# Performance work log

Hardware: AMD Instinct MI355X
Metric: run time of the kernel (lower is better)

The kernel has to match this reference:

```python
import jax, jax.numpy as jnp
import numpy as np

V, E, H = 100000, 300, 256          # pretrained vectors, emb_dim, rep_dim
B, QLEN, DOC, S = 32, 32, 2048, 64  # batch, max_query_len, max_doc_len, max_num_sent
L = DOC // S                        # sentence length (lengths sum exactly to DOC)
VOCAB = V + 2                       # + extra token + padding idx


def _uniform(k, shape, scale):
    return jax.random.uniform(k, shape, jnp.float32, -scale, scale)


def setup_inputs() -> dict:
    key = jax.random.key(0)
    ks = jax.random.split(key, 16)
    s = 1.0 / np.sqrt(H)  # PyTorch GRU default init scale
    return {
        "queries": jax.random.randint(ks[0], (B, QLEN), 0, V),
        "query_lengths": jax.random.randint(ks[1], (B,), QLEN // 2, QLEN + 1).astype(jnp.int32),
        "docs": jax.random.randint(ks[2], (B, DOC), 0, V),
        "sentence_lengths": jnp.full((B, S), L, dtype=jnp.int32),
        "emb": jax.random.normal(ks[3], (VOCAB, E), jnp.float32) * 0.1,
        "q_wih": _uniform(ks[4], (3 * H, E), s), "q_whh": _uniform(ks[5], (3 * H, H), s),
        "q_bih": _uniform(ks[6], (3 * H,), s), "q_bhh": _uniform(ks[7], (3 * H,), s),
        "f_wih": _uniform(ks[8], (3 * H, E), s), "f_whh": _uniform(ks[9], (3 * H, H), s),
        "f_bih": _uniform(ks[10], (3 * H,), s), "f_bhh": _uniform(ks[11], (3 * H,), s),
        "b_wih": _uniform(ks[12], (3 * H, E), s), "b_whh": _uniform(ks[13], (3 * H, H), s),
        "b_bih": _uniform(ks[14], (3 * H,), s), "b_bhh": _uniform(ks[15], (3 * H,), s),
    }


def _gru(x, wih, whh, bih, bhh, reverse=False):
    # x: (B, T, E) -> hidden states (B, T, H); PyTorch GRU cell equations.
    xg = jnp.einsum('bte,ge->btg', x, wih) + bih  # (B, T, 3H) input projections

    def step(h, xt):
        gh = h @ whh.T + bhh
        ir, iz, inn = jnp.split(xt, 3, axis=-1)
        hr, hz, hn = jnp.split(gh, 3, axis=-1)
        r = jax.nn.sigmoid(ir + hr)
        z = jax.nn.sigmoid(iz + hz)
        n = jnp.tanh(inn + r * hn)
        hnew = (1.0 - z) * n + z * h
        return hnew, hnew

    h0 = jnp.zeros((x.shape[0], whh.shape[1]), x.dtype)
    _, hs = jax.lax.scan(step, h0, jnp.swapaxes(xg, 0, 1), reverse=reverse)
    return jnp.swapaxes(hs, 0, 1)


def reference(queries, query_lengths, docs, sentence_lengths, emb,
              q_wih, q_whh, q_bih, q_bhh,
              f_wih, f_whh, f_bih, f_bhh,
              b_wih, b_whh, b_bih, b_bhh):
    q_emb = emb[queries]  # (B, QLEN, E)
    d_emb = emb[docs]     # (B, DOC, E)

    # Ragged per-sentence mean pooling (_get_facts) as one segment-mean per doc.
    def seg_mean(xb, lens):
        ids = jnp.repeat(jnp.arange(S), lens, total_repeat_length=DOC)
        sums = jax.ops.segment_sum(xb, ids, num_segments=S)
        return sums / jnp.maximum(lens, 1)[:, None].astype(xb.dtype)

    facts = jax.vmap(seg_mean)(d_emb, sentence_lengths)  # (B, S, E)

    # Question GRU: hidden state at the last valid token (pack_padded semantics).
    q_hs = _gru(q_emb, q_wih, q_whh, q_bih, q_bhh)
    q_rep = q_hs[jnp.arange(B), query_lengths - 1][:, None, :]  # (B, 1, H)

    # Input fusion: bidirectional GRU over facts, fwd + bwd halves summed (dropout off / eval).
    f_out = (_gru(facts, f_wih, f_whh, f_bih, f_bhh)
             + _gru(facts, b_wih, b_whh, b_bih, b_bhh, reverse=True))  # (B, S, H)

    num_facts = jnp.sum(sentence_lengths > 0, axis=1)
    return q_rep, f_out, num_facts
```

## Files before the change

kernel.cpp:

```cpp
#include <hip/hip_runtime.h>

#define Bn   32
#define QL   32
#define DOCn 2048
#define Sn   64
#define En   300
#define Hn   256

typedef short bf16x8 __attribute__((ext_vector_type(8)));
typedef short s16x4  __attribute__((ext_vector_type(4)));
typedef float f32x4  __attribute__((ext_vector_type(4)));

static __device__ __forceinline__ float b2f(short s){
  unsigned int u = ((unsigned int)(unsigned short)s) << 16;
  float f; __builtin_memcpy(&f, &u, 4); return f;
}
static __device__ __forceinline__ short f2b(float f){
  unsigned int u; __builtin_memcpy(&u, &f, 4);
  u = u + 0x7fffu + ((u >> 16) & 1u);
  return (short)(u >> 16);
}
static __device__ __forceinline__ float sigm(float x){ return 1.0f/(1.0f+__expf(-x)); }
static __device__ __forceinline__ float tanhx(float x){ return 1.0f - 2.0f/(__expf(2.0f*x)+1.0f); }
static __device__ __forceinline__ f32x4 mfma16(bf16x8 a, bf16x8 b, f32x4 c){
  return __builtin_amdgcn_mfma_f32_16x16x32_bf16(a, b, c, 0, 0, 0);
}
static __device__ __forceinline__ void bar_lgkm(){
  asm volatile("s_waitcnt lgkmcnt(0)\n\ts_barrier" ::: "memory");
}

__global__ __launch_bounds__(256) void k_facts(
    const int* __restrict__ docs, const int* __restrict__ slens,
    const float* __restrict__ emb,
    const float* __restrict__ f_wih, const float* __restrict__ b_wih,
    const float* __restrict__ q_wih,
    short* __restrict__ facts, short* __restrict__ wcvt,
    float* __restrict__ dout)
{
  const int tid = threadIdx.x;

  if (blockIdx.x >= 2048){
    const int rg0 = (blockIdx.x - 2048)*8;
#pragma unroll
    for (int rr = 0; rr < 8; ++rr){
      const int rg = rg0 + rr;
      const int z = rg / 768, g = rg % 768;
      const float* src = ((z == 0) ? f_wih : (z == 1) ? b_wih : q_wih) + (long)g*En;
      short* dst = wcvt + (long)rg*320;
      for (int c = tid; c < 320; c += 256)
        dst[c] = (c < En) ? f2b(src[c]) : (short)0;
    }
    return;
  }

  __shared__ int pref[2*Sn];
  const int blk = blockIdx.x;
  const int b = blk >> 6, s = blk & 63;
  if (tid < Sn){
    const int v = slens[b*Sn + tid];
    int x = v;
#pragma unroll
    for (int d = 1; d < 64; d <<= 1){
      const int y = __shfl_up(x, d, 64);
      if (tid >= d) x += y;
    }
    pref[tid] = x - v;
    pref[Sn + tid] = v;
    if (s == 0){
      const unsigned long long m = __ballot(v > 0);
      if (tid == 0) dout[Bn*Hn + (long)Bn*Sn*Hn + b] = (float)__popcll(m);
    }
  }
  __syncthreads();
  const int off = pref[s];
  const int len = pref[Sn + s];
  const bool act = tid < 150;
  float a0 = 0.f, a1 = 0.f, b0 = 0.f, b1 = 0.f;
  const int* dtok = docs + b*DOCn + off;
  int tkA = (0 < len) ? dtok[0] : 0;
  int tkB = (1 < len) ? dtok[1] : 0;
  int i = 0;
  for (; i + 2 <= len; i += 2){
    const int tkA2 = (i+2 < len) ? dtok[i+2] : 0;
    const int tkB2 = (i+3 < len) ? dtok[i+3] : 0;
    if (act){
      const float2 va = *(const float2*)(emb + (long)tkA*En + 2*tid);
      const float2 vb = *(const float2*)(emb + (long)tkB*En + 2*tid);
      a0 += va.x; a1 += va.y; b0 += vb.x; b1 += vb.y;
    }
    tkA = tkA2; tkB = tkB2;
  }
  if (i < len && act){
    const float2 va = *(const float2*)(emb + (long)tkA*En + 2*tid);
    a0 += va.x; a1 += va.y;
  }
  a0 += b0; a1 += b1;
  const float inv = 1.0f / (float)(len > 0 ? len : 1);
  short* frow = facts + ((long)b*Sn + s)*320;
  if (act){
    frow[2*tid]   = f2b(a0*inv);
    frow[2*tid+1] = f2b(a1*inv);
  } else if (tid < 160){
    const int e = tid - 150;
    frow[300 + 2*e] = 0; frow[301 + 2*e] = 0;
  }
}

__global__ __launch_bounds__(256) void k_xg(
    const short* __restrict__ facts, const short* __restrict__ wcvt,
    const int* __restrict__ queries, const float* __restrict__ emb,
    const float* __restrict__ q_bih, const float* __restrict__ q_bhh,
    const float* __restrict__ f_bih, const float* __restrict__ f_bhh,
    const float* __restrict__ b_bih, const float* __restrict__ b_bhh,
    short* __restrict__ q_xgi, short* __restrict__ f_xgi,
    short* __restrict__ b_xgi)
{
  const int z = blockIdx.z;
  const int bm = blockIdx.x, bn = blockIdx.y;
  const bool isq = (z == 2);
  if (isq && bm >= 8) return;

  const float* bih = (z == 0) ? f_bih : (z == 1) ? b_bih : q_bih;
  const float* bhh = (z == 0) ? f_bhh : (z == 1) ? b_bhh : q_bhh;
  short*       xgi = (z == 0) ? f_xgi : (z == 1) ? b_xgi : q_xgi;

  __shared__ alignas(16) short Al[2][128][40];
  const int tid = threadIdx.x;
  const int l = tid & 63, w = tid >> 6;
  const int wm = w & 1, wn = w >> 1;
  const int l15 = l & 15, lq = l >> 4;
  const int ak8 = w*8;

  bf16x8 bfr[2][10];
#pragma unroll
  for (int nt = 0; nt < 2; ++nt){
    const int g = bn*64 + wn*32 + nt*16 + l15;
    const short* wr = wcvt + ((long)z*768 + g)*320;
#pragma unroll
    for (int kk = 0; kk < 10; ++kk)
      bfr[nt][kk] = *(const bf16x8*)&wr[kk*32 + lq*8];
  }

  const short* asrc_f0 = nullptr; const short* asrc_f1 = nullptr;
  const float* asrc_q0 = nullptr; const float* asrc_q1 = nullptr;
  if (isq){
    asrc_q0 = emb + (long)queries[bm*128 + l]*En;
    asrc_q1 = emb + (long)queries[bm*128 + 64 + l]*En;
  } else {
    asrc_f0 = facts + (long)(bm*128 + l)*320;
    asrc_f1 = facts + (long)(bm*128 + 64 + l)*320;
  }

  bf16x8 va0, va1;
#define LDA_(KK) do{ const int k0_ = (KK)*32 + ak8; \
    if (!isq){ \
      va0 = *(const bf16x8*)(asrc_f0 + k0_); \
      va1 = *(const bf16x8*)(asrc_f1 + k0_); \
    } else if (k0_ + 7 < En){ \
      const f32x4 p0 = *(const f32x4*)(asrc_q0+k0_), p1 = *(const f32x4*)(asrc_q0+k0_+4); \
      const f32x4 p2 = *(const f32x4*)(asrc_q1+k0_), p3 = *(const f32x4*)(asrc_q1+k0_+4); \
      _Pragma("unroll") for (int j = 0; j < 4; ++j){ \
        va0[j] = f2b(p0[j]); va0[4+j] = f2b(p1[j]); \
        va1[j] = f2b(p2[j]); va1[4+j] = f2b(p3[j]); } \
    } else { \
      _Pragma("unroll") for (int j = 0; j < 8; ++j){ const int k_ = k0_ + j; \
        va0[j] = (k_ < En) ? f2b(asrc_q0[k_]) : (short)0; \
        va1[j] = (k_ < En) ? f2b(asrc_q1[k_]) : (short)0; } \
    } }while(0)
#define STA_(BUF) do{ *(bf16x8*)&Al[BUF][l][ak8] = va0; \
    *(bf16x8*)&Al[BUF][64 + l][ak8] = va1; }while(0)

  LDA_(0); STA_(0);
  __syncthreads();

  f32x4 acc[4][2] = {};
#pragma unroll
  for (int kk = 0; kk < 10; ++kk){
    if (kk < 9) LDA_(kk+1);
#pragma unroll
    for (int mt = 0; mt < 4; ++mt){
      bf16x8 a = *(const bf16x8*)&Al[kk&1][wm*64 + mt*16 + l15][lq*8];
      acc[mt][0] = mfma16(a, bfr[0][kk], acc[mt][0]);
      acc[mt][1] = mfma16(a, bfr[1][kk], acc[mt][1]);
    }
    if (kk < 9) STA_((kk+1)&1);
    __syncthreads();
  }
#undef LDA_
#undef STA_

#pragma unroll
  for (int nt = 0; nt < 2; ++nt){
    const int cg = bn*64 + wn*32 + nt*16 + l15;
    float bias = bih[cg];
    if (cg < 512) bias += bhh[cg];
    const int gate = cg >> 8, hc = cg & 255;
    const int wslot = (hc >> 4)*64 + (hc & 15);
#pragma unroll
    for (int mt = 0; mt < 4; ++mt){
      const int r0 = bm*128 + wm*64 + mt*16 + lq*4;
#pragma unroll
      for (int p = 0; p < 4; ++p){
        const int r = r0 + p;
        const int t_ = isq ? (r & 31) : (r & 63);
        const int b_ = isq ? (r >> 5) : (r >> 6);
        const int mh_ = b_ >> 4, rb = b_ & 15;
        const long sidx = (long)t_*32768 + mh_*16384
                        + (long)(wslot + (rb >> 2)*16)*16 + (rb & 3)*3 + gate;
        xgi[sidx] = f2b(acc[mt][nt][p] + bias);
      }
    }
  }
}

__global__ __launch_bounds__(1024) void k_gru(
    const short* __restrict__ q_xg, const short* __restrict__ f_xg,
    const short* __restrict__ b_xg,
    const float* __restrict__ q_whh, const float* __restrict__ q_bhh,
    const float* __restrict__ f_whh, const float* __restrict__ f_bhh,
    const float* __restrict__ b_whh, const float* __restrict__ b_bhh,
    const int* __restrict__ qlens,
    float* __restrict__ dout)
{
  __shared__ alignas(16) short hl[2*16*264];
  __shared__ alignas(16) short wl[7*1024*8];

  const int gru = blockIdx.x >> 1;
  const int mh  = blockIdx.x & 1;
  const int tid = threadIdx.x;
  const int l = tid & 63, w = tid >> 6;
  const int l15 = l & 15, lq = l >> 4;

  const float* whh = (gru == 0) ? q_whh : (gru == 1) ? f_whh : b_whh;
  const float* bhh = (gru == 0) ? q_bhh : (gru == 1) ? f_bhh : b_bhh;
  const short* xgp = (gru == 0) ? q_xg  : (gru == 1) ? f_xg  : b_xg;
  const int T = (gru == 0) ? QL : Sn;

  const int c = w*16 + l15;

  bf16x8 wf[3][6];
  float bhn = 0.f;
#pragma unroll
  for (int gi = 0; gi < 3; ++gi){
    const int g = gi*256 + c;
    const float* wr = whh + (long)g*Hn;
#pragma unroll
    for (int kk = 0; kk < 8; ++kk){
      const f32x4 f0 = *(const f32x4*)(wr + kk*32 + lq*8);
      const f32x4 f1 = *(const f32x4*)(wr + kk*32 + lq*8 + 4);
      bf16x8 v;
#pragma unroll
      for (int j = 0; j < 4; ++j){ v[j] = f2b(f0[j]); v[4+j] = f2b(f1[j]); }
      if (kk < 5 || (kk == 5 && gi < 2)) wf[gi][kk] = v;
      else if (kk == 5)                  *(bf16x8*)&wl[(6*1024 + tid)*8] = v;
      else                               *(bf16x8*)&wl[(((kk-6)*3 + gi)*1024 + tid)*8] = v;
    }
    if (gi == 2) bhn = bhh[g];
  }

  float hreg[4] = {};
  int qlen_m[4];
#pragma unroll
  for (int p = 0; p < 4; ++p) qlen_m[p] = (gru == 0) ? qlens[mh*16 + lq*4 + p] : -1;

  const int so = mh*16384 + tid*16;
  float* qdst  = dout + (mh*16 + lq*4)*Hn + c;
  float* fbase = dout + Bn*Hn + (long)(mh*16 + lq*4)*(Sn*Hn) + c;

  bf16x8 preA0, preA1, preB0, preB1;

#define TOF(TT) ((gru == 2) ? (T - 1 - (TT)) : (TT))
#define LOADP(P0, P1, TI) do{ const short* sb_ = xgp + (long)(TI)*32768 + so; \
    P0 = *(const bf16x8*)(sb_); P1 = *(const bf16x8*)(sb_ + 8); }while(0)

#define GRU_EW(P, HOUT, IRV, IZV, INV) do{ \
      const float ir = b2f(IRV), iz = b2f(IZV), in_ = b2f(INV); \
      const float rr = sigm(ir + acc0[P]); \
      const float zz = sigm(iz + acc1[P]); \
      const float nn = tanhx(in_ + rr*acc2[P]); \
      const float hn = (1.0f - zz)*nn + zz*hreg[P]; \
      hreg[P] = hn; \
      (HOUT)[(lq*4 + P)*264 + c] = f2b(hn); \
      if (gru == 0){ if (t_ == qlen_m[P] - 1) qdst[P*Hn] = hn; } \
      else { atomicAdd(fbase + P*(Sn*Hn) + t_*Hn, hn); } \
    }while(0)

#define GRU_STEP(TT, DOM, HIN, HOUT, PR0, PR1) do{ \
    f32x4 acc0 = (f32x4){0.f,0.f,0.f,0.f}; \
    f32x4 acc1 = (f32x4){0.f,0.f,0.f,0.f}; \
    f32x4 acc2 = (f32x4){bhn,bhn,bhn,bhn}; \
    if (DOM){ \
      _Pragma("unroll") for (int kk = 0; kk < 5; ++kk){ \
        const bf16x8 a = *(const bf16x8*)&(HIN)[l15*264 + kk*32 + lq*8]; \
        acc0 = mfma16(a, wf[0][kk], acc0); \
        acc1 = mfma16(a, wf[1][kk], acc1); \
        acc2 = mfma16(a, wf[2][kk], acc2); \
      } \
      { const bf16x8 a = *(const bf16x8*)&(HIN)[l15*264 + 5*32 + lq*8]; \
        const bf16x8 w2 = *(const bf16x8*)&wl[(6*1024 + tid)*8]; \
        acc0 = mfma16(a, wf[0][5], acc0); \
        acc1 = mfma16(a, wf[1][5], acc1); \
        acc2 = mfma16(a, w2, acc2); } \
      { const bf16x8 a = *(const bf16x8*)&(HIN)[l15*264 + 6*32 + lq*8]; \
        const bf16x8 w0 = *(const bf16x8*)&wl[(0*1024 + tid)*8]; \
        const bf16x8 w1 = *(const bf16x8*)&wl[(1*1024 + tid)*8]; \
        const bf16x8 w2 = *(const bf16x8*)&wl[(2*1024 + tid)*8]; \
        acc0 = mfma16(a, w0, acc0); \
        acc1 = mfma16(a, w1, acc1); \
        acc2 = mfma16(a, w2, acc2); } \
      { const bf16x8 a = *(const bf16x8*)&(HIN)[l15*264 + 7*32 + lq*8]; \
        const bf16x8 w0 = *(const bf16x8*)&wl[(3*1024 + tid)*8]; \
        const bf16x8 w1 = *(const bf16x8*)&wl[(4*1024 + tid)*8]; \
        const bf16x8 w2 = *(const bf16x8*)&wl[(5*1024 + tid)*8]; \
        acc0 = mfma16(a, w0, acc0); \
        acc1 = mfma16(a, w1, acc1); \
        acc2 = mfma16(a, w2, acc2); } \
    } \
    const int t_ = TOF(TT); \
    GRU_EW(0, HOUT, PR0[0], PR0[1], PR0[2]); \
    GRU_EW(1, HOUT, PR0[3], PR0[4], PR0[5]); \
    GRU_EW(2, HOUT, PR0[6], PR0[7], PR1[0]); \
    GRU_EW(3, HOUT, PR1[1], PR1[2], PR1[3]); \
  }while(0)

  short* h0 = hl;
  short* h1 = hl + 4224;

  LOADP(preA0, preA1, TOF(0));
  LOADP(preB0, preB1, TOF(1));
  __builtin_amdgcn_sched_barrier(0);
  GRU_STEP(0, 0, h1, h0, preA0, preA1);
  bar_lgkm();
  LOADP(preA0, preA1, TOF(2));
  __builtin_amdgcn_sched_barrier(0);
  GRU_STEP(1, 1, h0, h1, preB0, preB1);
  bar_lgkm();

  for (int tt = 2; tt < T; tt += 2){
    const int tiB = (tt+1 < T) ? (tt+1) : (T-1);
    LOADP(preB0, preB1, TOF(tiB));
    __builtin_amdgcn_sched_barrier(0);
    GRU_STEP(tt, 1, h1, h0, preA0, preA1);
    bar_lgkm();
    const int tiA = (tt+2 < T) ? (tt+2) : (T-1);
    LOADP(preA0, preA1, TOF(tiA));
    __builtin_amdgcn_sched_barrier(0);
    GRU_STEP(tt+1, 1, h0, h1, preB0, preB1);
    bar_lgkm();
  }
#undef TOF
#undef LOADP
#undef GRU_EW
#undef GRU_STEP
}

extern "C" void kernel_launch(void* const* d_in, const int* in_sizes, int n_in,
                              void* d_out, int out_size, void* d_ws, size_t ws_size,
                              hipStream_t stream)
{
  const int*   queries = (const int*)d_in[0];
  const int*   qlens   = (const int*)d_in[1];
  const int*   docs    = (const int*)d_in[2];
  const int*   slens   = (const int*)d_in[3];
  const float* emb     = (const float*)d_in[4];
  const float* q_wih   = (const float*)d_in[5];
  const float* q_whh   = (const float*)d_in[6];
  const float* q_bih   = (const float*)d_in[7];
  const float* q_bhh   = (const float*)d_in[8];
  const float* f_wih   = (const float*)d_in[9];
  const float* f_whh   = (const float*)d_in[10];
  const float* f_bih   = (const float*)d_in[11];
  const float* f_bhh   = (const float*)d_in[12];
  const float* b_wih   = (const float*)d_in[13];
  const float* b_whh   = (const float*)d_in[14];
  const float* b_bih   = (const float*)d_in[15];
  const float* b_bhh   = (const float*)d_in[16];

  char* wsb = (char*)d_ws;
  short* f_xgi = (short*)(wsb);
  short* b_xgi = (short*)(wsb +  4194304);
  short* q_xgi = (short*)(wsb +  8388608);
  short* facts = (short*)(wsb + 10485760);
  short* wcvt  = (short*)(wsb + 11796480);

  float* dout = (float*)d_out;

  k_facts<<<dim3(2048 + 288), 256, 0, stream>>>(docs, slens, emb,
                                                f_wih, b_wih, q_wih,
                                                facts, wcvt, dout);
  k_xg   <<<dim3(16, 12, 3), 256, 0, stream>>>(facts, wcvt, queries, emb,
                                               q_bih, q_bhh, f_bih, f_bhh,
                                               b_bih, b_bhh,
                                               q_xgi, f_xgi, b_xgi);
  k_gru  <<<dim3(6), 1024, 0, stream>>>(q_xgi, f_xgi, b_xgi, q_whh, q_bhh,
                                        f_whh, f_bhh, b_whh, b_bhh,
                                        qlens, dout);
}
```

Baseline: 482.0 us.

## Split GRU hidden dimension across paired workgroups with global-memory flag exchange

The recurrent GRU kernel now uses 12 workgroups of 512 threads instead of 6 of 1024. Each pair of workgroups owns half of the hidden columns, so all recurrent weights fit in registers and the LDS weight spill goes away. After each step the two halves swap their new hidden-state halves through a global buffer, with release/acquire flags and a spin-wait. The aim is to spread the serial recurrence over more CUs and cut per-step LDS traffic, at the cost of a cross-workgroup handshake every timestep and a reliance on paired blocks being co-resident.

```diff
diff --git a/kernel.cpp b/kernel.cpp
--- a/kernel.cpp
+++ b/kernel.cpp
@@ -35,11 +35,12 @@
     const float* __restrict__ f_wih, const float* __restrict__ b_wih,
     const float* __restrict__ q_wih,
     short* __restrict__ facts, short* __restrict__ wcvt,
-    float* __restrict__ dout)
+    int* __restrict__ flags, float* __restrict__ dout)
 {
   const int tid = threadIdx.x;
 
   if (blockIdx.x >= 2048){
+    if (blockIdx.x == 2048 && tid < 12) flags[tid] = 0;
     const int rg0 = (blockIdx.x - 2048)*8;
 #pragma unroll
     for (int rr = 0; rr < 8; ++rr){
@@ -213,20 +214,23 @@
   }
 }
 
-__global__ __launch_bounds__(1024) void k_gru(
+__global__ __launch_bounds__(512, 2) void k_gru(
     const short* __restrict__ q_xg, const short* __restrict__ f_xg,
     const short* __restrict__ b_xg,
     const float* __restrict__ q_whh, const float* __restrict__ q_bhh,
     const float* __restrict__ f_whh, const float* __restrict__ f_bhh,
     const float* __restrict__ b_whh, const float* __restrict__ b_bhh,
     const int* __restrict__ qlens,
+    short* __restrict__ xbuf, int* __restrict__ flags,
     float* __restrict__ dout)
 {
   __shared__ alignas(16) short hl[2*16*264];
-  __shared__ alignas(16) short wl[7*1024*8];
-
-  const int gru = blockIdx.x >> 1;
-  const int mh  = blockIdx.x & 1;
+
+  const int bid = blockIdx.x;
+  const int gru = bid >> 2;
+  const int mh  = (bid >> 1) & 1;
+  const int ch  = bid & 1;
+  const int pr  = gru*2 + mh;
   const int tid = threadIdx.x;
   const int l = tid & 63, w = tid >> 6;
   const int l15 = l & 15, lq = l >> 4;
@@ -236,9 +240,9 @@
   const short* xgp = (gru == 0) ? q_xg  : (gru == 1) ? f_xg  : b_xg;
   const int T = (gru == 0) ? QL : Sn;
 
-  const int c = w*16 + l15;
-
-  bf16x8 wf[3][6];
+  const int c = ch*128 + w*16 + l15;
+
+  bf16x8 wf[3][8];
   float bhn = 0.f;
 #pragma unroll
   for (int gi = 0; gi < 3; ++gi){
@@ -251,9 +255,7 @@
       bf16x8 v;
 #pragma unroll
       for (int j = 0; j < 4; ++j){ v[j] = f2b(f0[j]); v[4+j] = f2b(f1[j]); }
-      if (kk < 5 || (kk == 5 && gi < 2)) wf[gi][kk] = v;
-      else if (kk == 5)                  *(bf16x8*)&wl[(6*1024 + tid)*8] = v;
-      else                               *(bf16x8*)&wl[(((kk-6)*3 + gi)*1024 + tid)*8] = v;
+      wf[gi][kk] = v;
     }
     if (gi == 2) bhn = bhh[g];
   }
@@ -263,9 +265,17 @@
 #pragma unroll
   for (int p = 0; p < 4; ++p) qlen_m[p] = (gru == 0) ? qlens[mh*16 + lq*4 + p] : -1;
 
-  const int so = mh*16384 + tid*16;
+  const int so = mh*16384 + (((ch*8 + w)*64 + l))*16;
   float* qdst  = dout + (mh*16 + lq*4)*Hn + c;
   float* fbase = dout + Bn*Hn + (long)(mh*16 + lq*4)*(Sn*Hn) + c;
+
+  short* xw = xbuf + (pr*2 + ch)*4096;
+  const short* xr = xbuf + (pr*2 + (ch^1))*4096;
+  int* myflag = flags + pr*2 + ch;
+  int* pflag  = flags + pr*2 + (ch^1);
+  const int xr_row = tid >> 5;
+  const int xr_c4  = (tid & 31)*4;
+  const int pcol   = (ch^1)*128;
 
   bf16x8 preA0, preA1, preB0, preB1;
 
@@ -273,84 +283,80 @@
 #define LOADP(P0, P1, TI) do{ const short* sb_ = xgp + (long)(TI)*32768 + so; \
     P0 = *(const bf16x8*)(sb_); P1 = *(const bf16x8*)(sb_ + 8); }while(0)
 
-#define GRU_EW(P, HOUT, IRV, IZV, INV) do{ \
+#define EWC(P, IRV, IZV, INV) \
+    float hn##P; { \
       const float ir = b2f(IRV), iz = b2f(IZV), in_ = b2f(INV); \
       const float rr = sigm(ir + acc0[P]); \
       const float zz = sigm(iz + acc1[P]); \
       const float nn = tanhx(in_ + rr*acc2[P]); \
-      const float hn = (1.0f - zz)*nn + zz*hreg[P]; \
-      hreg[P] = hn; \
-      (HOUT)[(lq*4 + P)*264 + c] = f2b(hn); \
-      if (gru == 0){ if (t_ == qlen_m[P] - 1) qdst[P*Hn] = hn; } \
-      else { atomicAdd(fbase + P*(Sn*Hn) + t_*Hn, hn); } \
-    }while(0)
-
-#define GRU_STEP(TT, DOM, HIN, HOUT, PR0, PR1) do{ \
+      hn##P = (1.0f - zz)*nn + zz*hreg[P]; \
+      hreg[P] = hn##P; }
+
+#define GRU_STEP(TT, DOM, DOEX, HIN, HOUT, PR0, PR1, PN0, PN1) do{ \
     f32x4 acc0 = (f32x4){0.f,0.f,0.f,0.f}; \
     f32x4 acc1 = (f32x4){0.f,0.f,0.f,0.f}; \
     f32x4 acc2 = (f32x4){bhn,bhn,bhn,bhn}; \
     if (DOM){ \
-      _Pragma("unroll") for (int kk = 0; kk < 5; ++kk){ \
+      _Pragma("unroll") for (int kk = 0; kk < 8; ++kk){ \
         const bf16x8 a = *(const bf16x8*)&(HIN)[l15*264 + kk*32 + lq*8]; \
         acc0 = mfma16(a, wf[0][kk], acc0); \
         acc1 = mfma16(a, wf[1][kk], acc1); \
         acc2 = mfma16(a, wf[2][kk], acc2); \
       } \
-      { const bf16x8 a = *(const bf16x8*)&(HIN)[l15*264 + 5*32 + lq*8]; \
-        const bf16x8 w2 = *(const bf16x8*)&wl[(6*1024 + tid)*8]; \
-        acc0 = mfma16(a, wf[0][5], acc0); \
-        acc1 = mfma16(a, wf[1][5], acc1); \
-        acc2 = mfma16(a, w2, acc2); } \
-      { const bf16x8 a = *(const bf16x8*)&(HIN)[l15*264 + 6*32 + lq*8]; \
-        const bf16x8 w0 = *(const bf16x8*)&wl[(0*1024 + tid)*8]; \
-        const bf16x8 w1 = *(const bf16x8*)&wl[(1*1024 + tid)*8]; \
-        const bf16x8 w2 = *(const bf16x8*)&wl[(2*1024 + tid)*8]; \
-        acc0 = mfma16(a, w0, acc0); \
-        acc1 = mfma16(a, w1, acc1); \
-        acc2 = mfma16(a, w2, acc2); } \
-      { const bf16x8 a = *(const bf16x8*)&(HIN)[l15*264 + 7*32 + lq*8]; \
-        const bf16x8 w0 = *(const bf16x8*)&wl[(3*1024 + tid)*8]; \
-        const bf16x8 w1 = *(const bf16x8*)&wl[(4*1024 + tid)*8]; \
-        const bf16x8 w2 = *(const bf16x8*)&wl[(5*1024 + tid)*8]; \
-        acc0 = mfma16(a, w0, acc0); \
-        acc1 = mfma16(a, w1, acc1); \
-        acc2 = mfma16(a, w2, acc2); } \
     } \
     const int t_ = TOF(TT); \
-    GRU_EW(0, HOUT, PR0[0], PR0[1], PR0[2]); \
-    GRU_EW(1, HOUT, PR0[3], PR0[4], PR0[5]); \
-    GRU_EW(2, HOUT, PR0[6], PR0[7], PR1[0]); \
-    GRU_EW(3, HOUT, PR1[1], PR1[2], PR1[3]); \
+    EWC(0, PR0[0], PR0[1], PR0[2]); \
+    EWC(1, PR0[3], PR0[4], PR0[5]); \
+    EWC(2, PR0[6], PR0[7], PR1[0]); \
+    EWC(3, PR1[1], PR1[2], PR1[3]); \
+    if (DOEX){ \
+      short* xwb = xw + ((TT)&1)*2048 + (lq*4)*128 + (c & 127); \
+      xwb[0]   = f2b(hn0); xwb[128] = f2b(hn1); \
+      xwb[256] = f2b(hn2); xwb[384] = f2b(hn3); \
+      __hip_atomic_store(myflag, (TT)+1, __ATOMIC_RELEASE, __HIP_MEMORY_SCOPE_AGENT); \
+      __builtin_amdgcn_sched_barrier(0); \
+      LOADP(PN0, PN1, TOF((TT)+1)); \
+    } \
+    (HOUT)[(lq*4+0)*264 + c] = f2b(hn0); \
+    (HOUT)[(lq*4+1)*264 + c] = f2b(hn1); \
+    (HOUT)[(lq*4+2)*264 + c] = f2b(hn2); \
+    (HOUT)[(lq*4+3)*264 + c] = f2b(hn3); \
+    if (gru == 0){ \
+      if (t_ == qlen_m[0]-1) qdst[0*Hn] = hn0; \
+      if (t_ == qlen_m[1]-1) qdst[1*Hn] = hn1; \
+      if (t_ == qlen_m[2]-1) qdst[2*Hn] = hn2; \
+      if (t_ == qlen_m[3]-1) qdst[3*Hn] = hn3; \
+    } else { \
+      atomicAdd(fbase + 0*(Sn*Hn) + t_*Hn, hn0); \
+      atomicAdd(fbase + 1*(Sn*Hn) + t_*Hn, hn1); \
+      atomicAdd(fbase + 2*(Sn*Hn) + t_*Hn, hn2); \
+      atomicAdd(fbase + 3*(Sn*Hn) + t_*Hn, hn3); \
+    } \
+    if (DOEX){ \
+      const int want_ = (TT) + 1; \
+      while (__hip_atomic_load(pflag, __ATOMIC_ACQUIRE, __HIP_MEMORY_SCOPE_AGENT) < want_) \
+        __builtin_amdgcn_s_sleep(2); \
+      const s16x4 pv = *(const s16x4*)&xr[((TT)&1)*2048 + xr_row*128 + xr_c4]; \
+      *(s16x4*)&(HOUT)[xr_row*264 + pcol + xr_c4] = pv; \
+    } \
+    bar_lgkm(); \
   }while(0)
 
   short* h0 = hl;
   short* h1 = hl + 4224;
 
   LOADP(preA0, preA1, TOF(0));
-  LOADP(preB0, preB1, TOF(1));
   __builtin_amdgcn_sched_barrier(0);
-  GRU_STEP(0, 0, h1, h0, preA0, preA1);
-  bar_lgkm();
-  LOADP(preA0, preA1, TOF(2));
-  __builtin_amdgcn_sched_barrier(0);
-  GRU_STEP(1, 1, h0, h1, preB0, preB1);
-  bar_lgkm();
-
-  for (int tt = 2; tt < T; tt += 2){
-    const int tiB = (tt+1 < T) ? (tt+1) : (T-1);
-    LOADP(preB0, preB1, TOF(tiB));
-    __builtin_amdgcn_sched_barrier(0);
-    GRU_STEP(tt, 1, h1, h0, preA0, preA1);
-    bar_lgkm();
-    const int tiA = (tt+2 < T) ? (tt+2) : (T-1);
-    LOADP(preA0, preA1, TOF(tiA));
-    __builtin_amdgcn_sched_barrier(0);
-    GRU_STEP(tt+1, 1, h0, h1, preB0, preB1);
-    bar_lgkm();
-  }
+  GRU_STEP(0, 0, 1, h1, h0, preA0, preA1, preB0, preB1);
+
+  for (int tt = 1; tt + 1 < T; tt += 2){
+    GRU_STEP(tt,   1, 1, h0, h1, preB0, preB1, preA0, preA1);
+    GRU_STEP(tt+1, 1, 1, h1, h0, preA0, preA1, preB0, preB1);
+  }
+  GRU_STEP(T-1, 1, 0, h0, h1, preB0, preB1, preA0, preA1);
 #undef TOF
 #undef LOADP
-#undef GRU_EW
+#undef EWC
 #undef GRU_STEP
 }
 
@@ -382,17 +388,19 @@
   short* q_xgi = (short*)(wsb +  8388608);
   short* facts = (short*)(wsb + 10485760);
   short* wcvt  = (short*)(wsb + 11796480);
+  short* xbuf  = (short*)(wsb + 13271040);
+  int*   flags = (int*)  (wsb + 13369344);
 
   float* dout = (float*)d_out;
 
   k_facts<<<dim3(2048 + 288), 256, 0, stream>>>(docs, slens, emb,
                                                 f_wih, b_wih, q_wih,
-                                                facts, wcvt, dout);
+                                                facts, wcvt, flags, dout);
   k_xg   <<<dim3(16, 12, 3), 256, 0, stream>>>(facts, wcvt, queries, emb,
                                                q_bih, q_bhh, f_bih, f_bhh,
                                                b_bih, b_bhh,
                                                q_xgi, f_xgi, b_xgi);
-  k_gru  <<<dim3(6), 1024, 0, stream>>>(q_xgi, f_xgi, b_xgi, q_whh, q_bhh,
+  k_gru  <<<dim3(12), 512, 0, stream>>>(q_xgi, f_xgi, b_xgi, q_whh, q_bhh,
                                         f_whh, f_bhh, b_whh, b_bhh,
-                                        qlens, dout);
-}
+                                        qlens, xbuf, flags, dout);
+}
```

Measured after the change: 611.1 us. 1.27x slower.
